# Performance work log

Hardware: AMD Instinct MI355X
Metric: run time of the kernel (lower is better)

## Reference

```python
import jax, jax.numpy as jnp
import numpy as np
import math

B, T, C, H = 4, 2048, 1024, 16

def setup_inputs() -> dict:
    key = jax.random.key(0)
    k1, k2, k3 = jax.random.split(key, 3)
    scale = 1.0 / math.sqrt(C)
    return {
        "x": jax.random.normal(k1, (B, T, C), dtype=jnp.float32),
        "w_attn": jax.random.normal(k2, (C, 3 * C), dtype=jnp.float32) * scale,
        "b_attn": jnp.zeros((3 * C,), dtype=jnp.float32),
        "w_proj": jax.random.normal(k3, (C, C), dtype=jnp.float32) * scale,
        "b_proj": jnp.zeros((C,), dtype=jnp.float32),
    }

def reference(x, w_attn, b_attn, w_proj, b_proj):
    Bq, Tq, Cq = x.shape
    hd = Cq // H  # head dim
    qkv = x @ w_attn + b_attn                       # [B,T,3C]
    q, k, v = jnp.split(qkv, 3, axis=-1)
    # [B,T,C] -> [B,H,T,hd]
    q = q.reshape(Bq, Tq, H, hd).transpose(0, 2, 1, 3)
    k = k.reshape(Bq, Tq, H, hd).transpose(0, 2, 1, 3)
    v = v.reshape(Bq, Tq, H, hd).transpose(0, 2, 1, 3)
    att = jnp.einsum('bhqd,bhkd->bhqk', q, k) * (1.0 / math.sqrt(hd))
    causal = jnp.tril(jnp.ones((Tq, Tq), dtype=bool))
    att = jnp.where(causal[None, None], att, -jnp.inf)
    att = jax.nn.softmax(att, axis=-1)              # dropout p=0 (eval)
    y = jnp.einsum('bhqk,bhkd->bhqd', att, v)       # [B,H,T,hd]
    y = y.transpose(0, 2, 1, 3).reshape(Bq, Tq, Cq)
    return y @ w_proj + b_proj
```

## Files before the change

### kernel.cpp

```cpp
#include <hip/hip_runtime.h>


#define T_SEQ 2048
#define NB 4
#define NH 16
#define CDIM 1024
#define HD 64
#define BH (NB * NH)
#define QSCALE 0.1803368801111204f

typedef float f32x4 __attribute__((ext_vector_type(4)));
typedef float f32x16 __attribute__((ext_vector_type(16)));
typedef __bf16 bf16x8 __attribute__((ext_vector_type(8)));
typedef unsigned short u16x8 __attribute__((ext_vector_type(8)));
typedef unsigned short u16x4 __attribute__((ext_vector_type(4)));

__device__ __forceinline__ unsigned short f2b(float f) {
    union { float f; unsigned u; } v; v.f = f;
    unsigned u = v.u;
    u += 0x7FFFu + ((u >> 16) & 1u);
    return (unsigned short)(u >> 16);
}

__device__ __forceinline__ f32x4 fzero4() {
    f32x4 z; z[0] = 0.f; z[1] = 0.f; z[2] = 0.f; z[3] = 0.f; return z;
}

__device__ __forceinline__ f32x4 mfma16(bf16x8 a, bf16x8 b, f32x4 c) {
    return __builtin_amdgcn_mfma_f32_16x16x32_bf16(a, b, c, 0, 0, 0);
}

__device__ __forceinline__ f32x16 mfma32(bf16x8 a, bf16x8 b, f32x16 c) {
    return __builtin_amdgcn_mfma_f32_32x32x16_bf16(a, b, c, 0, 0, 0);
}

__device__ __forceinline__ void gld16(const void* gp, void* lp) {
    __builtin_amdgcn_global_load_lds(
        (const __attribute__((address_space(1))) unsigned int*)gp,
        (__attribute__((address_space(3))) unsigned int*)lp, 16, 0, 0);
}

#define FENCE asm volatile("" ::: "memory")

__global__ __launch_bounds__(256) void cast_f32_bf16_kernel(
        const float* __restrict__ in, unsigned short* __restrict__ out, int n8) {
    int i = blockIdx.x * 256 + threadIdx.x;
    int stride = gridDim.x * 256;
    for (; i < n8; i += stride) {
        const float4* p = reinterpret_cast<const float4*>(in) + (size_t)i * 2;
        float4 a = p[0], b = p[1];
        u16x8 o;
        o[0] = f2b(a.x); o[1] = f2b(a.y); o[2] = f2b(a.z); o[3] = f2b(a.w);
        o[4] = f2b(b.x); o[5] = f2b(b.y); o[6] = f2b(b.z); o[7] = f2b(b.w);
        *(reinterpret_cast<u16x8*>(out) + i) = o;
    }
}

__global__ __launch_bounds__(256) void transpose_cast_kernel(
        const float* __restrict__ in, unsigned short* __restrict__ out, int R, int C) {
    __shared__ unsigned short tile[32][33];
    int tx = threadIdx.x, ty = threadIdx.y;
    int c0 = blockIdx.x * 32, r0 = blockIdx.y * 32;
    for (int rr = ty; rr < 32; rr += 8)
        tile[rr][tx] = f2b(in[(size_t)(r0 + rr) * C + c0 + tx]);
    __syncthreads();
    for (int rr = ty; rr < 32; rr += 8)
        out[(size_t)(c0 + rr) * R + r0 + tx] = tile[tx][rr];
}

template <int EPI>
__global__ __launch_bounds__(256) void gemm_bt_kernel(
        const unsigned short* __restrict__ A, const unsigned short* __restrict__ Bt,
        const float* __restrict__ bias, float* __restrict__ outF,
        unsigned short* __restrict__ q_out, unsigned short* __restrict__ k_out,
        unsigned short* __restrict__ v_out, int M, int N, int K) {
    __shared__ alignas(16) unsigned short As[2][128 * 32];
    __shared__ alignas(16) unsigned short Bs[2][128 * 32];

    int tid = threadIdx.x;
    int wid = tid >> 6, lane = tid & 63;
    int g = lane >> 4, lc = lane & 15;
    int wr = (wid >> 1) * 64, wc = (wid & 1) * 64;
    int m0 = blockIdx.y * 128, n0 = blockIdx.x * 128;

    f32x4 acc[4][4];
#pragma unroll
    for (int m = 0; m < 4; ++m)
#pragma unroll
        for (int n = 0; n < 4; ++n) acc[m][n] = fzero4();

    int srow = tid >> 2;
    int scol = ((tid & 3) ^ (srow & 3)) * 8;
    const unsigned short* Ap = A + (size_t)(m0 + srow) * K + scol;
    const unsigned short* Bp = Bt + (size_t)(n0 + srow) * K + scol;
    int ldst = (wid * 16) * 32;
    int ldst2 = (64 + wid * 16) * 32;

#define GSTAGE(BUF, KOFF)                                      \
    gld16(Ap + (KOFF), &As[BUF][ldst]);                        \
    gld16(Ap + (size_t)64 * K + (KOFF), &As[BUF][ldst2]);      \
    gld16(Bp + (KOFF), &Bs[BUF][ldst]);                        \
    gld16(Bp + (size_t)64 * K + (KOFF), &Bs[BUF][ldst2]);

    GSTAGE(0, 0)
    GSTAGE(1, 32)

    int swz8 = (g ^ (lc & 3)) * 8;

    int nk = K >> 5;
    for (int it = 0; it < nk; ++it) {
        int cur = it & 1;
        if (it + 1 < nk) { asm volatile("s_waitcnt vmcnt(4)" ::: "memory"); }
        else             { asm volatile("s_waitcnt vmcnt(0)" ::: "memory"); }
        FENCE; __builtin_amdgcn_s_barrier(); FENCE;

        bf16x8 af[4], bfr[4];
#pragma unroll
        for (int m = 0; m < 4; ++m)
            af[m] = *(const bf16x8*)&As[cur][(wr + m * 16 + lc) * 32 + swz8];
#pragma unroll
        for (int n = 0; n < 4; ++n)
            bfr[n] = *(const bf16x8*)&Bs[cur][(wc + n * 16 + lc) * 32 + swz8];

        __builtin_amdgcn_s_setprio(1);
#pragma unroll
        for (int m = 0; m < 4; ++m)
#pragma unroll
            for (int n = 0; n < 4; ++n)
                acc[m][n] = mfma16(af[m], bfr[n], acc[m][n]);
        __builtin_amdgcn_s_setprio(0);

        FENCE; __builtin_amdgcn_s_barrier(); FENCE;
        if (it + 2 < nk) { GSTAGE(cur, (it + 2) << 5) }
    }
#undef GSTAGE

#pragma unroll
    for (int m = 0; m < 4; ++m) {
        int rowb = m0 + wr + m * 16 + g * 4;
#pragma unroll
        for (int n = 0; n < 4; ++n) {
            int col = n0 + wc + n * 16 + lc;
            float bv = bias[col];
            if (EPI == 0) {
#pragma unroll
                for (int i = 0; i < 4; ++i)
                    outF[(size_t)(rowb + i) * N + col] = acc[m][n][i] + bv;
            } else {
                int which = col >> 10;
                int c = col & 1023;
                int h = c >> 6, d = c & 63;
                int bh_ = (rowb >> 11) * NH + h;
                int tl = rowb & 2047;
                if (which == 2) {
                    u16x4 vq;
#pragma unroll
                    for (int i = 0; i < 4; ++i) vq[i] = f2b(acc[m][n][i] + bv);
                    *(u16x4*)&v_out[(size_t)bh_ * (HD * T_SEQ) + (size_t)d * T_SEQ + tl] = vq;
                } else {
                    unsigned short* dst = which ? k_out : q_out;
                    float sc = which ? 1.0f : QSCALE;
#pragma unroll
                    for (int i = 0; i < 4; ++i)
                        dst[((size_t)bh_ * T_SEQ + tl + i) * HD + d] =
                            f2b((acc[m][n][i] + bv) * sc);
                }
            }
        }
    }
}

__global__ __launch_bounds__(256, 4) void attn32_kernel(
        const unsigned short* __restrict__ Qb, const unsigned short* __restrict__ Kb,
        const unsigned short* __restrict__ Vt, unsigned short* __restrict__ Yb) {
    __shared__ alignas(16) char smem[32768];

    int tid = threadIdx.x;
    int wid = tid >> 6, lane = tid & 63;
    int ql = lane & 31, hi = lane >> 5;
    int ql7 = ql & 7;

    int id = blockIdx.x;
    int x = id & 7;
    int k = id >> 3;
    int r = k >> 5;
    int c = k & 31;
    int hh = 2 * r + (c >> 4);
    int j = c & 15;
    int qg = (r & 1) ? (15 - j) : j;
    int bh = x * 8 + hh;
    size_t hb = (size_t)bh * (T_SEQ * HD);

    int qt = qg * 4 + wid;
    int q0 = qt * 32;
    int ktMax = qt >> 1;
    int ntB = 2 * qg + 2;

    bf16x8 qf[4];
    const unsigned short* Qp = Qb + hb + (size_t)(q0 + ql) * HD + hi * 8;
#pragma unroll
    for (int d = 0; d < 4; ++d) qf[d] = *(const bf16x8*)(Qp + d * 16);

    f32x16 zz;
#pragma unroll
    for (int rr = 0; rr < 16; ++rr) zz[rr] = 0.f;
    f32x16 o0 = zz, o1 = zz;
    float mi = -__builtin_inff(), li = 0.f;

    int r8 = lane >> 3;
    int sslot8 = ((lane & 7) ^ r8) * 8;
    const unsigned short* Kg = Kb + hb + (size_t)(wid * 16 + r8) * HD + sslot8;
    const unsigned short* Vg = Vt + hb + (size_t)(wid * 16 + r8) * T_SEQ + sslot8;

    gld16(Kg, smem + wid * 2048);
    gld16(Kg + 8 * HD, smem + wid * 2048 + 1024);
    gld16(Vg, smem + 8192 + wid * 2048);
    gld16(Vg + 8 * T_SEQ, smem + 8192 + wid * 2048 + 1024);
    __syncthreads();

#define KF(K0, D) (*(const bf16x8*)&KB_[(((K0)*32 + ql) << 6) + ((((D)*2 + hi) ^ ql7) << 3)])
#define VF(DB, T) (*(const bf16x8*)&VB_[(((DB)*32 + ql) << 6) + ((((T)*2 + hi) ^ ql7) << 3)])

    for (int kt = 0; kt < ntB; ++kt) {
        int cur = kt & 1;
        if (kt + 1 < ntB) {
            char* nb = smem + (cur ^ 1) * 16384;
            gld16(Kg + (size_t)(kt + 1) * 64 * HD, nb + wid * 2048);
            gld16(Kg + (size_t)((kt + 1) * 64 + 8) * HD, nb + wid * 2048 + 1024);
            gld16(Vg + (kt + 1) * 64, nb + 8192 + wid * 2048);
            gld16(Vg + (kt + 1) * 64 + 8 * T_SEQ, nb + 8192 + wid * 2048 + 1024);
        }
        if (kt <= ktMax) {
            const unsigned short* KB_ = (const unsigned short*)(smem + cur * 16384);
            const unsigned short* VB_ = (const unsigned short*)(smem + cur * 16384 + 8192);
            int k0 = kt * 64;

            f32x16 s0_, s1_;
            __builtin_amdgcn_s_setprio(1);
            s0_ = mfma32(KF(0, 0), qf[0], zz);
            s0_ = mfma32(KF(0, 1), qf[1], s0_);
            s0_ = mfma32(KF(0, 2), qf[2], s0_);
            s0_ = mfma32(KF(0, 3), qf[3], s0_);
            s1_ = mfma32(KF(1, 0), qf[0], zz);
            s1_ = mfma32(KF(1, 1), qf[1], s1_);
            s1_ = mfma32(KF(1, 2), qf[2], s1_);
            s1_ = mfma32(KF(1, 3), qf[3], s1_);
            __builtin_amdgcn_s_setprio(0);

            if (kt == ktMax) {
                int qg_ = q0 + ql;
#pragma unroll
                for (int rr = 0; rr < 16; ++rr) {
                    int kof_ = k0 + 8 * (rr >> 2) + (rr & 3) + 4 * hi;
                    if (kof_ > qg_) s0_[rr] = -__builtin_inff();
                    if (kof_ + 32 > qg_) s1_[rr] = -__builtin_inff();
                }
            }

            float t_[8];
#pragma unroll
            for (int rr = 0; rr < 8; ++rr)
                t_[rr] = fmaxf(fmaxf(s0_[rr], s0_[rr + 8]), fmaxf(s1_[rr], s1_[rr + 8]));
#pragma unroll
            for (int rr = 0; rr < 4; ++rr) t_[rr] = fmaxf(t_[rr], t_[rr + 4]);
            float pm_ = fmaxf(fmaxf(t_[0], t_[1]), fmaxf(t_[2], t_[3]));
            pm_ = fmaxf(pm_, __shfl_xor(pm_, 32));

            float mn_ = mi;
            if (!__all((int)(pm_ <= mi + 8.f))) {
                mn_ = fmaxf(mi, pm_);
                float f_ = __builtin_amdgcn_exp2f(mi - mn_);
                mi = mn_;
                li *= f_;
                o0 *= f_;
                o1 *= f_;
            }
#pragma unroll
            for (int rr = 0; rr < 16; ++rr) {
                s0_[rr] = __builtin_amdgcn_exp2f(s0_[rr] - mn_);
                s1_[rr] = __builtin_amdgcn_exp2f(s1_[rr] - mn_);
            }
            float u_[8];
#pragma unroll
            for (int rr = 0; rr < 8; ++rr)
                u_[rr] = (s0_[rr] + s0_[rr + 8]) + (s1_[rr] + s1_[rr + 8]);
#pragma unroll
            for (int rr = 0; rr < 4; ++rr) u_[rr] += u_[rr + 4];
            float ps_ = (u_[0] + u_[1]) + (u_[2] + u_[3]);
            ps_ += __shfl_xor(ps_, 32);
            li += ps_;

#pragma unroll
            for (int K0_ = 0; K0_ < 2; ++K0_) {
#pragma unroll
                for (int h2_ = 0; h2_ < 2; ++h2_) {
                    float e0_ = K0_ ? s1_[8 * h2_ + 0] : s0_[8 * h2_ + 0];
                    float e1_ = K0_ ? s1_[8 * h2_ + 1] : s0_[8 * h2_ + 1];
                    float e2_ = K0_ ? s1_[8 * h2_ + 2] : s0_[8 * h2_ + 2];
                    float e3_ = K0_ ? s1_[8 * h2_ + 3] : s0_[8 * h2_ + 3];
                    float e4_ = K0_ ? s1_[8 * h2_ + 4] : s0_[8 * h2_ + 4];
                    float e5_ = K0_ ? s1_[8 * h2_ + 5] : s0_[8 * h2_ + 5];
                    float e6_ = K0_ ? s1_[8 * h2_ + 6] : s0_[8 * h2_ + 6];
                    float e7_ = K0_ ? s1_[8 * h2_ + 7] : s0_[8 * h2_ + 7];
                    unsigned a_, b_, c_, d_;
                    asm("v_cvt_pk_bf16_f32 %0, %1, %2" : "=v"(a_) : "v"(e0_), "v"(e1_));
                    asm("v_cvt_pk_bf16_f32 %0, %1, %2" : "=v"(b_) : "v"(e2_), "v"(e3_));
                    asm("v_cvt_pk_bf16_f32 %0, %1, %2" : "=v"(c_) : "v"(e4_), "v"(e5_));
                    asm("v_cvt_pk_bf16_f32 %0, %1, %2" : "=v"(d_) : "v"(e6_), "v"(e7_));
                    asm("v_permlane32_swap_b32 %0, %1" : "+v"(a_), "+v"(c_));
                    asm("v_permlane32_swap_b32 %0, %1" : "+v"(b_), "+v"(d_));
                    union { unsigned u[4]; bf16x8 v; } pf_;
                    pf_.u[0] = a_; pf_.u[1] = b_; pf_.u[2] = c_; pf_.u[3] = d_;
                    __builtin_amdgcn_s_setprio(1);
                    o0 = mfma32(VF(0, K0_ * 2 + h2_), pf_.v, o0);
                    o1 = mfma32(VF(1, K0_ * 2 + h2_), pf_.v, o1);
                    __builtin_amdgcn_s_setprio(0);
                }
            }
        }
        __syncthreads();
    }
#undef KF
#undef VF

    int bb = bh >> 4, h = bh & 15;
    float iv = 1.0f / li;
#pragma unroll
    for (int dblk = 0; dblk < 2; ++dblk) {
#pragma unroll
        for (int a = 0; a < 4; ++a) {
            u16x4 wv;
#pragma unroll
            for (int i = 0; i < 4; ++i)
                wv[i] = f2b((dblk ? o1[4 * a + i] : o0[4 * a + i]) * iv);
            int dq = dblk * 32 + 8 * a + 4 * hi;
            *(u16x4*)&Yb[((size_t)(bb * T_SEQ + q0 + ql)) * CDIM + h * HD + dq] = wv;
        }
    }
}

extern "C" void kernel_launch(void* const* d_in, const int* in_sizes, int n_in,
                              void* d_out, int out_size, void* d_ws, size_t ws_size,
                              hipStream_t stream) {
    const float* x      = (const float*)d_in[0];
    const float* w_attn = (const float*)d_in[1];
    const float* b_attn = (const float*)d_in[2];
    const float* w_proj = (const float*)d_in[3];
    const float* b_proj = (const float*)d_in[4];
    float* out = (float*)d_out;

    char* ws = (char*)d_ws;
    unsigned short* xb  = (unsigned short*)(ws);
    unsigned short* wTa = (unsigned short*)(ws + 16777216);
    unsigned short* wTp = (unsigned short*)(ws + 23068672);
    unsigned short* qb  = (unsigned short*)(ws + 25165824);
    unsigned short* kb  = (unsigned short*)(ws + 41943040);
    unsigned short* vTb = (unsigned short*)(ws + 58720256);
    unsigned short* yb  = xb;

    cast_f32_bf16_kernel<<<2048, 256, 0, stream>>>(x, xb, (NB * T_SEQ * CDIM) / 8);
    transpose_cast_kernel<<<dim3(3072 / 32, 1024 / 32), dim3(32, 8), 0, stream>>>(
        w_attn, wTa, 1024, 3072);
    transpose_cast_kernel<<<dim3(1024 / 32, 1024 / 32), dim3(32, 8), 0, stream>>>(
        w_proj, wTp, 1024, 1024);

    gemm_bt_kernel<1><<<dim3(3072 / 128, 8192 / 128), 256, 0, stream>>>(
        xb, wTa, b_attn, nullptr, qb, kb, vTb, 8192, 3072, 1024);

    attn32_kernel<<<dim3(1024), 256, 0, stream>>>(qb, kb, vTb, yb);

    gemm_bt_kernel<0><<<dim3(1024 / 128, 8192 / 128), 256, 0, stream>>>(
        yb, wTp, b_proj, out, nullptr, nullptr, nullptr, 8192, 1024, 1024);
}
```

Baseline: 173.2 us.

## Merge prep kernels, single-buffer A in QKV GEMM, split attention barriers

The three cast/transpose launches become one prep kernel that dispatches on block index, removing two kernel launches. The QKV GEMM is split out and keeps A in a single LDS buffer, cutting shared memory to allow more resident blocks, at the cost of loading A only one step ahead. The attention loop now waits on vmcnt and barriers at the top of each tile instead of one __syncthreads at the end, overlapping the next tile's prefetch with the current tile's wait. Single-buffered A reduces latency hiding in the GEMM.

```diff
diff --git a/kernel.cpp b/kernel.cpp
--- a/kernel.cpp
+++ b/kernel.cpp
@@ -42,39 +42,51 @@
 
 #define FENCE asm volatile("" ::: "memory")
 
-__global__ __launch_bounds__(256) void cast_f32_bf16_kernel(
-        const float* __restrict__ in, unsigned short* __restrict__ out, int n8) {
-    int i = blockIdx.x * 256 + threadIdx.x;
-    int stride = gridDim.x * 256;
-    for (; i < n8; i += stride) {
-        const float4* p = reinterpret_cast<const float4*>(in) + (size_t)i * 2;
-        float4 a = p[0], b = p[1];
-        u16x8 o;
-        o[0] = f2b(a.x); o[1] = f2b(a.y); o[2] = f2b(a.z); o[3] = f2b(a.w);
-        o[4] = f2b(b.x); o[5] = f2b(b.y); o[6] = f2b(b.z); o[7] = f2b(b.w);
-        *(reinterpret_cast<u16x8*>(out) + i) = o;
-    }
-}
-
-__global__ __launch_bounds__(256) void transpose_cast_kernel(
-        const float* __restrict__ in, unsigned short* __restrict__ out, int R, int C) {
+__device__ __forceinline__ void transpose_tile(
+        const float* __restrict__ in, unsigned short* __restrict__ out,
+        int R, int C, int bx, int by) {
     __shared__ unsigned short tile[32][33];
-    int tx = threadIdx.x, ty = threadIdx.y;
-    int c0 = blockIdx.x * 32, r0 = blockIdx.y * 32;
+    int tx = threadIdx.x & 31, ty = threadIdx.x >> 5;
+    int c0 = bx * 32, r0 = by * 32;
+#pragma unroll
     for (int rr = ty; rr < 32; rr += 8)
         tile[rr][tx] = f2b(in[(size_t)(r0 + rr) * C + c0 + tx]);
     __syncthreads();
+#pragma unroll
     for (int rr = ty; rr < 32; rr += 8)
         out[(size_t)(c0 + rr) * R + r0 + tx] = tile[tx][rr];
 }
 
-template <int EPI>
-__global__ __launch_bounds__(256) void gemm_bt_kernel(
+__global__ __launch_bounds__(256) void prep_kernel(
+        const float* __restrict__ x, const float* __restrict__ wa,
+        const float* __restrict__ wp, unsigned short* __restrict__ xb,
+        unsigned short* __restrict__ wTa, unsigned short* __restrict__ wTp) {
+    int b = blockIdx.x;
+    if (b < 1024) {
+        int n8 = (NB * T_SEQ * CDIM) / 8;
+        for (int i = b * 256 + threadIdx.x; i < n8; i += 1024 * 256) {
+            const float4* p = reinterpret_cast<const float4*>(x) + (size_t)i * 2;
+            float4 a = p[0], c = p[1];
+            u16x8 o;
+            o[0] = f2b(a.x); o[1] = f2b(a.y); o[2] = f2b(a.z); o[3] = f2b(a.w);
+            o[4] = f2b(c.x); o[5] = f2b(c.y); o[6] = f2b(c.z); o[7] = f2b(c.w);
+            *(reinterpret_cast<u16x8*>(xb) + i) = o;
+        }
+    } else if (b < 1024 + 3072) {
+        int t = b - 1024;
+        transpose_tile(wa, wTa, 1024, 3072, t % 96, t / 96);
+    } else {
+        int t = b - 4096;
+        transpose_tile(wp, wTp, 1024, 1024, t % 32, t / 32);
+    }
+}
+
+__global__ __launch_bounds__(256) void gemm_qkv_kernel(
         const unsigned short* __restrict__ A, const unsigned short* __restrict__ Bt,
-        const float* __restrict__ bias, float* __restrict__ outF,
+        const float* __restrict__ bias,
         unsigned short* __restrict__ q_out, unsigned short* __restrict__ k_out,
         unsigned short* __restrict__ v_out, int M, int N, int K) {
-    __shared__ alignas(16) unsigned short As[2][128 * 32];
+    __shared__ alignas(16) unsigned short As[128 * 32];
     __shared__ alignas(16) unsigned short Bs[2][128 * 32];
 
     int tid = threadIdx.x;
@@ -96,6 +108,104 @@
     int ldst = (wid * 16) * 32;
     int ldst2 = (64 + wid * 16) * 32;
 
+#define STAGE_A(KOFF) {                                    \
+        gld16(Ap + (KOFF), &As[ldst]);                     \
+        gld16(Ap + (size_t)64 * K + (KOFF), &As[ldst2]); }
+#define STAGE_B(BUF, KOFF) {                                       \
+        gld16(Bp + (KOFF), &Bs[BUF][ldst]);                        \
+        gld16(Bp + (size_t)64 * K + (KOFF), &Bs[BUF][ldst2]); }
+
+    STAGE_B(0, 0)
+    STAGE_A(0)
+    STAGE_B(1, 32)
+
+    int swz8 = (g ^ (lc & 3)) * 8;
+
+    int nk = K >> 5;
+    for (int it = 0; it < nk; ++it) {
+        if (it + 1 < nk) { asm volatile("s_waitcnt vmcnt(2)" ::: "memory"); }
+        else             { asm volatile("s_waitcnt vmcnt(0)" ::: "memory"); }
+        FENCE; __builtin_amdgcn_s_barrier(); FENCE;
+
+        bf16x8 af[4], bfr[4];
+        const unsigned short* Bb = Bs[it & 1];
+#pragma unroll
+        for (int m = 0; m < 4; ++m)
+            af[m] = *(const bf16x8*)&As[(wr + m * 16 + lc) * 32 + swz8];
+#pragma unroll
+        for (int n = 0; n < 4; ++n)
+            bfr[n] = *(const bf16x8*)&Bb[(wc + n * 16 + lc) * 32 + swz8];
+
+        __builtin_amdgcn_s_setprio(1);
+#pragma unroll
+        for (int m = 0; m < 4; ++m)
+#pragma unroll
+            for (int n = 0; n < 4; ++n)
+                acc[m][n] = mfma16(af[m], bfr[n], acc[m][n]);
+        __builtin_amdgcn_s_setprio(0);
+
+        asm volatile("s_waitcnt lgkmcnt(0)" ::: "memory");
+        FENCE; __builtin_amdgcn_s_barrier(); FENCE;
+        if (it + 1 < nk) STAGE_A((it + 1) << 5)
+        if (it + 2 < nk) STAGE_B(it & 1, (it + 2) << 5)
+    }
+#undef STAGE_A
+#undef STAGE_B
+
+#pragma unroll
+    for (int m = 0; m < 4; ++m) {
+        int rowb = m0 + wr + m * 16 + g * 4;
+#pragma unroll
+        for (int n = 0; n < 4; ++n) {
+            int col = n0 + wc + n * 16 + lc;
+            float bv = bias[col];
+            int which = col >> 10;
+            int c = col & 1023;
+            int h = c >> 6, d = c & 63;
+            int bh_ = (rowb >> 11) * NH + h;
+            int tl = rowb & 2047;
+            if (which == 2) {
+                u16x4 vq;
+#pragma unroll
+                for (int i = 0; i < 4; ++i) vq[i] = f2b(acc[m][n][i] + bv);
+                *(u16x4*)&v_out[(size_t)bh_ * (HD * T_SEQ) + (size_t)d * T_SEQ + tl] = vq;
+            } else {
+                unsigned short* dst = which ? k_out : q_out;
+                float sc = which ? 1.0f : QSCALE;
+#pragma unroll
+                for (int i = 0; i < 4; ++i)
+                    dst[((size_t)bh_ * T_SEQ + tl + i) * HD + d] =
+                        f2b((acc[m][n][i] + bv) * sc);
+            }
+        }
+    }
+}
+
+__global__ __launch_bounds__(256) void gemm_proj_kernel(
+        const unsigned short* __restrict__ A, const unsigned short* __restrict__ Bt,
+        const float* __restrict__ bias, float* __restrict__ outF, int M, int N, int K) {
+    __shared__ alignas(16) unsigned short As[2][128 * 32];
+    __shared__ alignas(16) unsigned short Bs[2][128 * 32];
+
+    int tid = threadIdx.x;
+    int wid = tid >> 6, lane = tid & 63;
+    int g = lane >> 4, lc = lane & 15;
+    int wr = (wid >> 1) * 64, wc = (wid & 1) * 64;
+    int m0 = blockIdx.y * 128, n0 = blockIdx.x * 128;
+
+    f32x4 acc[4][4];
+#pragma unroll
+    for (int m = 0; m < 4; ++m)
+#pragma unroll
+        for (int n = 0; n < 4; ++n) acc[m][n] = fzero4();
+
+    int srow = tid >> 2;
+    int scol = ((tid & 3) ^ (srow & 3)) * 8;
+    const unsigned short* Ap = A + (size_t)(m0 + srow) * K + scol;
+    const unsigned short* Bp = Bt + (size_t)(n0 + srow) * K + scol;
+    int ldst = (wid * 16) * 32;
+    int ldst2 = (64 + wid * 16) * 32;
+
 #define GSTAGE(BUF, KOFF)                                      \
     gld16(Ap + (KOFF), &As[BUF][ldst]);                        \
     gld16(Ap + (size_t)64 * K + (KOFF), &As[BUF][ldst2]);      \
@@ -142,30 +252,9 @@
         for (int n = 0; n < 4; ++n) {
             int col = n0 + wc + n * 16 + lc;
             float bv = bias[col];
-            if (EPI == 0) {
-#pragma unroll
-                for (int i = 0; i < 4; ++i)
-                    outF[(size_t)(rowb + i) * N + col] = acc[m][n][i] + bv;
-            } else {
-                int which = col >> 10;
-                int c = col & 1023;
-                int h = c >> 6, d = c & 63;
-                int bh_ = (rowb >> 11) * NH + h;
-                int tl = rowb & 2047;
-                if (which == 2) {
-                    u16x4 vq;
-#pragma unroll
-                    for (int i = 0; i < 4; ++i) vq[i] = f2b(acc[m][n][i] + bv);
-                    *(u16x4*)&v_out[(size_t)bh_ * (HD * T_SEQ) + (size_t)d * T_SEQ + tl] = vq;
-                } else {
-                    unsigned short* dst = which ? k_out : q_out;
-                    float sc = which ? 1.0f : QSCALE;
-#pragma unroll
-                    for (int i = 0; i < 4; ++i)
-                        dst[((size_t)bh_ * T_SEQ + tl + i) * HD + d] =
-                            f2b((acc[m][n][i] + bv) * sc);
-                }
-            }
+#pragma unroll
+            for (int i = 0; i < 4; ++i)
+                outF[(size_t)(rowb + i) * N + col] = acc[m][n][i] + bv;
         }
     }
 }
@@ -223,13 +312,18 @@
 
     for (int kt = 0; kt < ntB; ++kt) {
         int cur = kt & 1;
-        if (kt + 1 < ntB) {
+        bool pf = (kt + 1 < ntB);
+        if (pf) {
             char* nb = smem + (cur ^ 1) * 16384;
             gld16(Kg + (size_t)(kt + 1) * 64 * HD, nb + wid * 2048);
             gld16(Kg + (size_t)((kt + 1) * 64 + 8) * HD, nb + wid * 2048 + 1024);
             gld16(Vg + (kt + 1) * 64, nb + 8192 + wid * 2048);
             gld16(Vg + (kt + 1) * 64 + 8 * T_SEQ, nb + 8192 + wid * 2048 + 1024);
         }
+        if (pf) { asm volatile("s_waitcnt vmcnt(4)" ::: "memory"); }
+        else    { asm volatile("s_waitcnt vmcnt(0)" ::: "memory"); }
+        FENCE; __builtin_amdgcn_s_barrier(); FENCE;
+
         if (kt <= ktMax) {
             const unsigned short* KB_ = (const unsigned short*)(smem + cur * 16384);
             const unsigned short* VB_ = (const unsigned short*)(smem + cur * 16384 + 8192);
@@ -318,7 +412,8 @@
                 }
             }
         }
-        __syncthreads();
+        asm volatile("s_waitcnt lgkmcnt(0)" ::: "memory");
+        FENCE; __builtin_amdgcn_s_barrier(); FENCE;
     }
 #undef KF
 #undef VF
@@ -358,17 +453,13 @@
     unsigned short* vTb = (unsigned short*)(ws + 58720256);
     unsigned short* yb  = xb;
 
-    cast_f32_bf16_kernel<<<2048, 256, 0, stream>>>(x, xb, (NB * T_SEQ * CDIM) / 8);
-    transpose_cast_kernel<<<dim3(3072 / 32, 1024 / 32), dim3(32, 8), 0, stream>>>(
-        w_attn, wTa, 1024, 3072);
-    transpose_cast_kernel<<<dim3(1024 / 32, 1024 / 32), dim3(32, 8), 0, stream>>>(
-        w_proj, wTp, 1024, 1024);
-
-    gemm_bt_kernel<1><<<dim3(3072 / 128, 8192 / 128), 256, 0, stream>>>(
-        xb, wTa, b_attn, nullptr, qb, kb, vTb, 8192, 3072, 1024);
+    prep_kernel<<<dim3(5120), 256, 0, stream>>>(x, w_attn, w_proj, xb, wTa, wTp);
+
+    gemm_qkv_kernel<<<dim3(3072 / 128, 8192 / 128), 256, 0, stream>>>(
+        xb, wTa, b_attn, qb, kb, vTb, 8192, 3072, 1024);
 
     attn32_kernel<<<dim3(1024), 256, 0, stream>>>(qb, kb, vTb, yb);
 
-    gemm_bt_kernel<0><<<dim3(1024 / 128, 8192 / 128), 256, 0, stream>>>(
-        yb, wTp, b_proj, out, nullptr, nullptr, nullptr, 8192, 1024, 1024);
-}
+    gemm_proj_kernel<<<dim3(1024 / 128, 8192 / 128), 256, 0, stream>>>(
+        yb, wTp, b_proj, out, 8192, 1024, 1024);
+}
```

Measured after the change: 168.8 us. 2.5% less time.
